# Optimization experiments

Measured on AMD Instinct MI355X. Metric: run time of the kernel, lower is better.

## Reference

```python
import jax, jax.numpy as jnp
import numpy as np

DEPTH = 4
EPS = 1e-5


def _bn(x, g, b):
    # training-mode BatchNorm over (B,H,W) per channel
    m = x.mean(axis=(0, 2, 3), keepdims=True)
    v = x.var(axis=(0, 2, 3), keepdims=True)
    return (x - m) * jax.lax.rsqrt(v + EPS) * g[None, :, None, None] + b[None, :, None, None]


def _conv_bn(x, w, g, b):
    # 1x1 conv (no bias) + BatchNorm
    y = jnp.einsum('bchw,oc->bohw', x, w)
    return _bn(y, g, b)


def _block_max_broadcast(x, gsz):
    # max over each (H/gsz, W/gsz) block of a gsz x gsz grid, broadcast back
    B, C, H, W = x.shape
    xr = x.reshape(B, C, gsz, H // gsz, gsz, W // gsz)
    m = xr.max(axis=(3, 5), keepdims=True)
    return jnp.broadcast_to(m, xr.shape).reshape(B, C, H, W)


def setup_inputs() -> dict:
    key = jax.random.key(0)
    ks = jax.random.split(key, 3)
    B, C, H, W = 4, 128, 256, 256
    x = jax.random.normal(ks[0], (B, C, H, W), dtype=jnp.float32)
    conv_w = jax.random.normal(ks[1], (DEPTH, C, C), dtype=jnp.float32) * 0.05
    conv_g = jnp.ones((DEPTH, C), dtype=jnp.float32)
    conv_b = jnp.zeros((DEPTH, C), dtype=jnp.float32)
    final_w = jax.random.normal(ks[2], (C, (DEPTH + 1) * C), dtype=jnp.float32) * 0.05
    final_g = jnp.ones((C,), dtype=jnp.float32)
    final_b = jnp.zeros((C,), dtype=jnp.float32)
    return {"x": x, "conv_w": conv_w, "conv_g": conv_g, "conv_b": conv_b,
            "final_w": final_w, "final_g": final_g, "final_b": final_b}


def reference(x, conv_w, conv_g, conv_b, final_w, final_g, final_b):
    # p[0]: identity; p[1+d]: block-max over 2^d x 2^d grid broadcast back, then 1x1 conv+BN
    p = [x]
    for d in range(DEPTH):
        pooled = _block_max_broadcast(x, 2 ** d)  # d=0 -> global max broadcast
        p.append(_conv_bn(pooled, conv_w[d], conv_g[d], conv_b[d]))
    out = jnp.concatenate(p, axis=1)  # [B, 5C, H, W]
    return _conv_bn(out, final_w, final_g, final_b)
```

## Files before the change

kernel.cpp:

```cpp
#include <hip/hip_runtime.h>
#include <hip/hip_bf16.h>
#include <math.h>
#include <float.h>

#define B_ 4
#define C_ 128
#define P_ 65536

#define M3_OFF      0
#define M2_OFF      32768
#define M1_OFF      40960
#define M0_OFF      43008
#define YBASE_      43520
#define SCALED_OFF  87040
#define SHIFTD_OFF  87552
#define CONTRIB_OFF 88064
#define S3_OFF      120832
#define SX_OFF      153600
#define G_OFF       154112
#define SCALEF_OFF  219648
#define SHIFTF_OFF  219776
#define MAXP_OFF    219904
#define SUMP_OFF    744192

using short8 = __attribute__((ext_vector_type(8))) short;
using f32x4 = __attribute__((ext_vector_type(4))) float;
using f32x16 = __attribute__((ext_vector_type(16))) float;

__device__ __forceinline__ int level_rel(int d) {
    return YBASE_ - 512 * (((1 << (2 * (d + 1))) - 1) / 3);
}

__device__ __forceinline__ unsigned int bfpair(float a, float b) {
    unsigned int ua = __float_as_uint(a), ub = __float_as_uint(b);
    ua = (ua + 0x7fffu + ((ua >> 16) & 1u)) >> 16;
    ub = (ub + 0x7fffu + ((ub >> 16) & 1u)) & 0xffff0000u;
    return ua | ub;
}

#define GLDS16(src, dst)                                                    \
    __builtin_amdgcn_global_load_lds(                                       \
        (const __attribute__((address_space(1))) unsigned int*)(src),       \
        (__attribute__((address_space(3))) unsigned int*)(dst), 16, 0, 0)

__global__ __launch_bounds__(256) void k_gram_pool(const float* __restrict__ x,
                                                   float* __restrict__ ws,
                                                   float* __restrict__ gpart) {
    __shared__ float tile[2][8192];
    int wg = blockIdx.x;
    int b = wg >> 7, rc = wg & 127;
    const float* xb = x + (size_t)b * C_ * P_ + (size_t)rc * 512;
    int t = threadIdx.x, l = t & 63, wv = t >> 6;
    int tr = (wv >> 1) * 64;
    int tcc = (wv & 1) * 64;
    bool doacc = ((wv & 1) == 0);

    f32x16 acc[2][2];
#pragma unroll
    for (int i = 0; i < 2; ++i)
#pragma unroll
        for (int j = 0; j < 2; ++j)
#pragma unroll
            for (int r = 0; r < 16; ++r) acc[i][j][r] = 0.f;
    float mxA[2][8], smA[2][8];
#pragma unroll
    for (int i = 0; i < 2; ++i)
#pragma unroll
        for (int j = 0; j < 8; ++j) { mxA[i][j] = -FLT_MAX; smA[i][j] = 0.f; }

#pragma unroll
    for (int i = 0; i < 8; ++i) {
        int row = wv * 32 + i * 4 + (l >> 4);
        int chunk = (l & 15) ^ (row & 15);
        GLDS16(xb + (size_t)row * P_ + chunk * 4, &tile[0][(wv * 32 + i * 4) * 64]);
    }
    __syncthreads();

#pragma unroll
    for (int s = 0; s < 8; ++s) {
        if (s < 7) {
#pragma unroll
            for (int i = 0; i < 8; ++i) {
                int row = wv * 32 + i * 4 + (l >> 4);
                int chunk = (l & 15) ^ (row & 15);
                GLDS16(xb + (size_t)row * P_ + (s + 1) * 64 + chunk * 4,
                       &tile[(s + 1) & 1][(wv * 32 + i * 4) * 64]);
            }
        }
        const float* tl = &tile[s & 1][0];
#pragma unroll
        for (int ks = 0; ks < 4; ++ks) {
            int jci = 2 * (s & 3) + (ks >> 1);
            int ch = ks * 4 + ((l >> 5) << 1);
            short8 fr[4];
#pragma unroll
            for (int fi = 0; fi < 4; ++fi) {
                int row = (fi < 2 ? tr : tcc) + (fi & 1) * 32 + (l & 31);
                int sw = row & 15;
                const float* p0 = tl + row * 64 + ((ch ^ sw) << 2);
                const float* p1 = tl + row * 64 + (((ch + 1) ^ sw) << 2);
                float4 v0 = *(const float4*)p0;
                float4 v1 = *(const float4*)p1;
                if (fi < 2 && doacc) {
                    mxA[fi][jci] = fmaxf(mxA[fi][jci],
                        fmaxf(fmaxf(fmaxf(v0.x, v0.y), fmaxf(v0.z, v0.w)),
                              fmaxf(fmaxf(v1.x, v1.y), fmaxf(v1.z, v1.w))));
                    smA[fi][jci] += ((v0.x + v0.y) + (v0.z + v0.w)) +
                                    ((v1.x + v1.y) + (v1.z + v1.w));
                }
                union { uint4 u; short8 s8; } cu;
                cu.u = make_uint4(bfpair(v0.x, v0.y), bfpair(v0.z, v0.w),
                                  bfpair(v1.x, v1.y), bfpair(v1.z, v1.w));
                fr[fi] = cu.s8;
            }
            acc[0][0] = __builtin_amdgcn_mfma_f32_32x32x16_bf16(fr[0], fr[2], acc[0][0], 0, 0, 0);
            acc[0][1] = __builtin_amdgcn_mfma_f32_32x32x16_bf16(fr[0], fr[3], acc[0][1], 0, 0, 0);
            acc[1][0] = __builtin_amdgcn_mfma_f32_32x32x16_bf16(fr[1], fr[2], acc[1][0], 0, 0, 0);
            acc[1][1] = __builtin_amdgcn_mfma_f32_32x32x16_bf16(fr[1], fr[3], acc[1][1], 0, 0, 0);
        }
        __syncthreads();
    }

    size_t gb = (size_t)wg * 16384;
#pragma unroll
    for (int i = 0; i < 2; ++i)
#pragma unroll
        for (int j = 0; j < 2; ++j)
#pragma unroll
            for (int r = 0; r < 16; ++r) {
                int row = tr + i * 32 + (r & 3) + 8 * (r >> 2) + 4 * (l >> 5);
                int col = tcc + j * 32 + (l & 31);
                gpart[gb + (size_t)row * 128 + col] = acc[i][j][r];
            }
    if (doacc) {
        int i3 = rc >> 4, rr = rc & 15;
#pragma unroll
        for (int half = 0; half < 2; ++half)
#pragma unroll
            for (int jc = 0; jc < 8; ++jc) {
                float m = mxA[half][jc], sv = smA[half][jc];
                m = fmaxf(m, __shfl_xor(m, 32));
                sv += __shfl_xor(sv, 32);
                if (l < 32) {
                    int c = tr + half * 32 + l;
                    size_t idx = ((size_t)(b * 128 + c) * 64 + i3 * 8 + jc) * 16 + rr;
                    ws[MAXP_OFF + idx] = m;
                    ws[SUMP_OFF + idx] = sv;
                }
            }
    }
}

__global__ __launch_bounds__(256) void k_reduceG(const float* __restrict__ gpart,
                                                 float* __restrict__ ws) {
    int tid = blockIdx.x * 256 + threadIdx.x;
    int b = tid >> 14, inner = tid & 16383;
    const float* p = gpart + (size_t)b * 128 * 16384 + inner;
    float s = 0.f;
    for (int r = 0; r < 128; ++r) s += p[(size_t)r * 16384];
    ws[G_OFF + tid] = s;
}

__global__ __launch_bounds__(256) void k_reduceMS(float* __restrict__ ws) {
    int bc = blockIdx.x;
    int t = threadIdx.x;
    int blk = t >> 2, q = t & 3;
    __shared__ float bm[64], bs[64];
    __shared__ float lv[24];
    __shared__ float sxr[8];
    {
        size_t base = (size_t)bc * 1024 + blk * 16 + q * 4;
        float4 mv = *(const float4*)(ws + MAXP_OFF + base);
        float4 sv = *(const float4*)(ws + SUMP_OFF + base);
        float m = fmaxf(fmaxf(mv.x, mv.y), fmaxf(mv.z, mv.w));
        float s = (sv.x + sv.y) + (sv.z + sv.w);
        m = fmaxf(m, __shfl_xor(m, 1)); s += __shfl_xor(s, 1);
        m = fmaxf(m, __shfl_xor(m, 2)); s += __shfl_xor(s, 2);
        if (q == 0) {
            bm[blk] = m;
            bs[blk] = s;
            ws[M3_OFF + (size_t)bc * 64 + blk] = m;
            ws[S3_OFF + (size_t)bc * 64 + blk] = s;
        }
    }
    __syncthreads();
    if (t < 8) {
        float sx = 0.f;
        for (int r = 0; r < 8; ++r) sx += bs[t * 8 + r];
        sxr[t] = sx;
    }
    if (t < 16) {
        int i2 = t >> 2, j2 = t & 3;
        float m = -FLT_MAX;
        for (int a = 0; a < 2; ++a)
            for (int b2 = 0; b2 < 2; ++b2)
                m = fmaxf(m, bm[(2 * i2 + a) * 8 + 2 * j2 + b2]);
        lv[t] = m;
        ws[M2_OFF + (size_t)bc * 16 + t] = m;
    }
    __syncthreads();
    if (t == 0) {
        float sx = 0.f;
        for (int r = 0; r < 8; ++r) sx += sxr[r];
        ws[SX_OFF + bc] = sx;
    }
    if (t < 4) {
        int i1 = t >> 1, j1 = t & 1;
        float m = -FLT_MAX;
        for (int a = 0; a < 2; ++a)
            for (int b2 = 0; b2 < 2; ++b2)
                m = fmaxf(m, lv[(2 * i1 + a) * 4 + 2 * j1 + b2]);
        lv[16 + t] = m;
        ws[M1_OFF + (size_t)bc * 4 + t] = m;
    }
    __syncthreads();
    if (t == 0)
        ws[M0_OFF + bc] = fmaxf(fmaxf(lv[16], lv[17]), fmaxf(lv[18], lv[19]));
}

__global__ __launch_bounds__(256) void k_conv_pool(const float* __restrict__ conv_w,
                                                   float* __restrict__ ws) {
    int bid = blockIdx.x;
    int d = bid >> 4, b = (bid >> 2) & 3, cchunk = bid & 3;
    int NB = 1 << (2 * d);
    int rel = level_rel(d);
    const float* Mb = ws + rel + (size_t)b * 128 * NB;
    float* Yb = ws + YBASE_ + rel + (size_t)b * 128 * NB;
    __shared__ float mlds[8192];
    int t = threadIdx.x;
    int tot = 128 * NB;
    for (int i = t; i < tot; i += 256) mlds[i] = Mb[i];
    __syncthreads();
    if (NB >= 4) {
        int nbq = NB >> 2;
        int nq = 32 * nbq;
        for (int qi = t; qi < nq; qi += 256) {
            int co = cchunk * 32 + (qi >> (2 * d - 2));
            int bq = qi & (nbq - 1);
            const float* wrow = conv_w + ((size_t)d * 128 + co) * 128;
            float a0 = 0.f, a1 = 0.f, a2 = 0.f, a3 = 0.f;
            for (int ci = 0; ci < 128; ++ci) {
                float4 mv = *(const float4*)(&mlds[ci * NB + bq * 4]);
                float wvv = wrow[ci];
                a0 = fmaf(wvv, mv.x, a0);
                a1 = fmaf(wvv, mv.y, a1);
                a2 = fmaf(wvv, mv.z, a2);
                a3 = fmaf(wvv, mv.w, a3);
            }
            float4 r;
            r.x = a0; r.y = a1; r.z = a2; r.w = a3;
            *(float4*)(&Yb[co * NB + bq * 4]) = r;
        }
    } else {
        for (int oi = t; oi < 32; oi += 256) {
            int co = cchunk * 32 + oi;
            const float* wrow = conv_w + (size_t)co * 128;
            float acc = 0.f;
            for (int ci = 0; ci < 128; ++ci) acc = fmaf(mlds[ci], wrow[ci], acc);
            Yb[co] = acc;
        }
    }
}

__global__ __launch_bounds__(256) void k_bnstats_d(const float* __restrict__ conv_g,
                                                   const float* __restrict__ conv_b,
                                                   float* __restrict__ ws) {
    int tid = blockIdx.x * 256 + threadIdx.x;
    if (tid >= 512) return;
    int d = tid >> 7, c = tid & 127;
    int NB = 1 << (2 * d);
    const float* Y = ws + YBASE_ + level_rel(d);
    int n = 4 * NB;
    float s = 0.f;
    for (int b = 0; b < 4; ++b)
        for (int k = 0; k < NB; ++k) s += Y[((size_t)b * 128 + c) * NB + k];
    float mean = s / (float)n;
    float v = 0.f;
    for (int b = 0; b < 4; ++b)
        for (int k = 0; k < NB; ++k) {
            float dd = Y[((size_t)b * 128 + c) * NB + k] - mean;
            v = fmaf(dd, dd, v);
        }
    float var = v / (float)n;
    float sc = conv_g[d * 128 + c] * rsqrtf(var + 1e-5f);
    ws[SCALED_OFF + tid] = sc;
    ws[SHIFTD_OFF + tid] = conv_b[d * 128 + c] - mean * sc;
}

__global__ __launch_bounds__(128) void k_contrib(const float* __restrict__ final_w,
                                                 float* __restrict__ ws) {
    int b = blockIdx.x >> 6, blk3 = blockIdx.x & 63;
    int i3 = blk3 >> 3, j3 = blk3 & 7;
    __shared__ float pn[512];
    int t = threadIdx.x;
    for (int k = t; k < 512; k += 128) {
        int d = k >> 7, c = k & 127;
        int sh = 3 - d;
        int blkd = (i3 >> sh) * (1 << d) + (j3 >> sh);
        int NB = 1 << (2 * d);
        float yv = ws[YBASE_ + level_rel(d) + ((size_t)b * 128 + c) * NB + blkd];
        pn[k] = yv * ws[SCALED_OFF + k] + ws[SHIFTD_OFF + k];
    }
    __syncthreads();
    const float* fw = final_w + (size_t)t * 640 + 128;
    float acc = 0.f;
#pragma unroll 8
    for (int k = 0; k < 512; k += 4) {
        float4 f = *(const float4*)(fw + k);
        acc = fmaf(pn[k], f.x, acc);
        acc = fmaf(pn[k + 1], f.y, acc);
        acc = fmaf(pn[k + 2], f.z, acc);
        acc = fmaf(pn[k + 3], f.w, acc);
    }
    ws[CONTRIB_OFF + ((size_t)b * 128 + t) * 64 + blk3] = acc;
}

__global__ __launch_bounds__(128) void k_stats(const float* __restrict__ final_w,
                                               const float* __restrict__ final_g,
                                               const float* __restrict__ final_b,
                                               float* __restrict__ ws) {
    int o = blockIdx.x, t = threadIdx.x;
    __shared__ __align__(16) float wlds[128];
    __shared__ __align__(16) float cvl[64];
    __shared__ float rbuf[4];
    wlds[t] = final_w[(size_t)o * 640 + t];
    __syncthreads();
    float SSQ = 0.f, SUM = 0.f;
    for (int b = 0; b < 4; ++b) {
        if (t < 64) cvl[t] = ws[CONTRIB_OFF + (size_t)(b * 128 + o) * 64 + t];
        __syncthreads();
        const float* Gb = ws + G_OFF + (size_t)b * 16384 + (size_t)t * 128;
        float a1 = 0.f;
#pragma unroll 8
        for (int k = 0; k < 128; k += 4) {
            float4 g = *(const float4*)(Gb + k);
            float4 w = *(const float4*)(&wlds[k]);
            a1 = fmaf(g.x, w.x, fmaf(g.y, w.y, fmaf(g.z, w.z, fmaf(g.w, w.w, a1))));
        }
        const float* S3p = ws + S3_OFF + (size_t)(b * 128 + t) * 64;
        float a2 = 0.f;
#pragma unroll 8
        for (int k = 0; k < 64; k += 4) {
            float4 sv = *(const float4*)(S3p + k);
            float4 cv = *(const float4*)(&cvl[k]);
            a2 = fmaf(sv.x, cv.x, fmaf(sv.y, cv.y, fmaf(sv.z, cv.z, fmaf(sv.w, cv.w, a2))));
        }
        float r1 = (a1 + 2.f * a2) * wlds[t];
        float r2 = wlds[t] * ws[SX_OFF + b * 128 + t];
        if (t < 64) {
            r1 += 1024.f * cvl[t] * cvl[t];
            r2 += 1024.f * cvl[t];
        }
#pragma unroll
        for (int k = 1; k < 64; k <<= 1) {
            r1 += __shfl_xor(r1, k);
            r2 += __shfl_xor(r2, k);
        }
        if ((t & 63) == 0) {
            rbuf[(t >> 6) * 2] = r1;
            rbuf[(t >> 6) * 2 + 1] = r2;
        }
        __syncthreads();
        SSQ += rbuf[0] + rbuf[2];
        SUM += rbuf[1] + rbuf[3];
        __syncthreads();
    }
    if (t == 0) {
        float mean = SUM / 262144.f;
        float var = SSQ / 262144.f - mean * mean;
        float sc = final_g[o] * rsqrtf(var + 1e-5f);
        ws[SCALEF_OFF + o] = sc;
        ws[SHIFTF_OFF + o] = final_b[o] - mean * sc;
    }
}

__global__ __launch_bounds__(256) void k_out(const float* __restrict__ x,
                                             const float* __restrict__ final_w,
                                             const float* __restrict__ ws,
                                             float* __restrict__ out) {
    __shared__ uint4 wtileq[2048];
    __shared__ float scl[128], shf[128], cvs[512];
    unsigned char* wtile = (unsigned char*)wtileq;
    int wgid = blockIdx.x;
    int b = wgid >> 9, pt = wgid & 511;
    int p0 = pt * 128;
    int t = threadIdx.x, l = t & 63, wv = t >> 6;
#pragma unroll
    for (int it = 0; it < 32; ++it) {
        int pid = it * 256 + t;
        int o = pid >> 6, cp = (pid & 63) * 2;
        float2 f = *(const float2*)(final_w + (size_t)o * 640 + cp);
        unsigned int u = bfpair(f.x, f.y);
        int wa = (o * 256 + cp * 2) ^ ((o & 7) << 4);
        *(unsigned int*)(wtile + wa) = u;
    }
    if (t < 128) {
        scl[t] = ws[SCALEF_OFF + t];
        shf[t] = ws[SHIFTF_OFF + t];
    }
    int i3 = pt >> 6, jb = (pt & 1) * 4;
    for (int q = t; q < 512; q += 256) {
        int o = q >> 2, jj = q & 3;
        cvs[q] = ws[CONTRIB_OFF + (size_t)(b * 128 + o) * 64 + i3 * 8 + jb + jj];
    }
    __syncthreads();

    const float* xb = x + (size_t)b * C_ * P_;
    int pw = p0 + wv * 32;
    f32x4 acc[8][2];
#pragma unroll
    for (int i = 0; i < 8; ++i) {
        acc[i][0] = (f32x4){0.f, 0.f, 0.f, 0.f};
        acc[i][1] = (f32x4){0.f, 0.f, 0.f, 0.f};
    }
#pragma unroll
    for (int ks = 0; ks < 4; ++ks) {
        short8 bf[2];
#pragma unroll
        for (int nt = 0; nt < 2; ++nt) {
            const float* xp = xb + (size_t)(ks * 32 + (l >> 4) * 8) * P_ + (pw + nt * 16 + (l & 15));
            float f0 = xp[0 * P_], f1 = xp[1 * P_], f2 = xp[2 * P_], f3 = xp[3 * P_];
            float f4 = xp[4 * P_], f5 = xp[5 * P_], f6 = xp[6 * P_], f7 = xp[7 * P_];
            union { uint4 u; short8 s; } cvtu;
            cvtu.u = make_uint4(bfpair(f0, f1), bfpair(f2, f3), bfpair(f4, f5), bfpair(f6, f7));
            bf[nt] = cvtu.s;
        }
#pragma unroll
        for (int mt = 0; mt < 8; ++mt) {
            int ra = ((mt * 16 + (l & 15)) * 256 + ks * 64 + (l >> 4) * 16) ^ ((l & 7) << 4);
            short8 af = *(const short8*)(wtile + ra);
            acc[mt][0] = __builtin_amdgcn_mfma_f32_16x16x32_bf16(af, bf[0], acc[mt][0], 0, 0, 0);
            acc[mt][1] = __builtin_amdgcn_mfma_f32_16x16x32_bf16(af, bf[1], acc[mt][1], 0, 0, 0);
        }
    }
#pragma unroll
    for (int mt = 0; mt < 8; ++mt)
#pragma unroll
        for (int nt = 0; nt < 2; ++nt) {
            int p = pw + nt * 16 + (l & 15);
            int jj = ((p & 255) >> 5) & 3;
#pragma unroll
            for (int r = 0; r < 4; ++r) {
                int o = mt * 16 + (l >> 4) * 4 + r;
                float z = acc[mt][nt][r] + cvs[o * 4 + jj];
                out[(size_t)(b * 128 + o) * P_ + p] = fmaf(z, scl[o], shf[o]);
            }
        }
}

extern "C" void kernel_launch(void* const* d_in, const int* in_sizes, int n_in,
                              void* d_out, int out_size, void* d_ws, size_t ws_size,
                              hipStream_t stream) {
    const float* x = (const float*)d_in[0];
    const float* conv_w = (const float*)d_in[1];
    const float* conv_g = (const float*)d_in[2];
    const float* conv_b = (const float*)d_in[3];
    const float* final_w = (const float*)d_in[4];
    const float* final_g = (const float*)d_in[5];
    const float* final_b = (const float*)d_in[6];
    float* out = (float*)d_out;
    float* ws = (float*)d_ws;

    k_gram_pool<<<512, 256, 0, stream>>>(x, ws, out);
    k_reduceG<<<256, 256, 0, stream>>>(out, ws);
    k_reduceMS<<<512, 256, 0, stream>>>(ws);
    k_conv_pool<<<64, 256, 0, stream>>>(conv_w, ws);
    k_bnstats_d<<<2, 256, 0, stream>>>(conv_g, conv_b, ws);
    k_contrib<<<B_ * 64, 128, 0, stream>>>(final_w, ws);
    k_stats<<<128, 128, 0, stream>>>(final_w, final_g, final_b, ws);
    k_out<<<2048, 256, 0, stream>>>(x, final_w, ws, out);
}
```

Before: 196.1 us.

## Use a four-slot LDS ring with three loads in flight in gram-pool kernel

Replaces the two-stage double buffer of 64-column tiles with a four-slot ring of 32-column tiles. Three tiles are prefetched ahead, and each step waits with explicit vmcnt counts and a single barrier instead of two syncthreads per step. The aim is to keep more global-to-LDS traffic in flight and hide memory latency behind the MFMA and reduction work. In exchange it doubles the number of pipeline steps and adds hand-tuned wait counts that must match the issue pattern exactly.

```diff
diff --git a/kernel.cpp b/kernel.cpp
--- a/kernel.cpp
+++ b/kernel.cpp
@@ -46,14 +46,15 @@
 __global__ __launch_bounds__(256) void k_gram_pool(const float* __restrict__ x,
                                                    float* __restrict__ ws,
                                                    float* __restrict__ gpart) {
-    __shared__ float tile[2][8192];
+    __shared__ float buf[4][4096];
     int wg = blockIdx.x;
     int b = wg >> 7, rc = wg & 127;
     const float* xb = x + (size_t)b * C_ * P_ + (size_t)rc * 512;
-    int t = threadIdx.x, l = t & 63, wv = t >> 6;
+    int t_ = threadIdx.x, l = t_ & 63, wv = t_ >> 6;
     int tr = (wv >> 1) * 64;
     int tcc = (wv & 1) * 64;
     bool doacc = ((wv & 1) == 0);
+    int lrow = l >> 3, lch = l & 7;
 
     f32x16 acc[2][2];
 #pragma unroll
@@ -68,45 +69,54 @@
 #pragma unroll
         for (int j = 0; j < 8; ++j) { mxA[i][j] = -FLT_MAX; smA[i][j] = 0.f; }
 
-#pragma unroll
-    for (int i = 0; i < 8; ++i) {
-        int row = wv * 32 + i * 4 + (l >> 4);
-        int chunk = (l & 15) ^ (row & 15);
-        GLDS16(xb + (size_t)row * P_ + chunk * 4, &tile[0][(wv * 32 + i * 4) * 64]);
-    }
-    __syncthreads();
-
-#pragma unroll
-    for (int s = 0; s < 8; ++s) {
-        if (s < 7) {
-#pragma unroll
-            for (int i = 0; i < 8; ++i) {
-                int row = wv * 32 + i * 4 + (l >> 4);
-                int chunk = (l & 15) ^ (row & 15);
-                GLDS16(xb + (size_t)row * P_ + (s + 1) * 64 + chunk * 4,
-                       &tile[(s + 1) & 1][(wv * 32 + i * 4) * 64]);
-            }
-        }
-        const float* tl = &tile[s & 1][0];
-#pragma unroll
-        for (int ks = 0; ks < 4; ++ks) {
-            int jci = 2 * (s & 3) + (ks >> 1);
+#define ISSUE(tt)                                                            \
+    do {                                                                     \
+        _Pragma("unroll") for (int i_ = 0; i_ < 4; ++i_) {                   \
+            int row_ = wv * 32 + i_ * 8 + lrow;                              \
+            int ch_ = lch ^ (row_ & 7);                                      \
+            GLDS16(xb + (size_t)row_ * P_ + (tt) * 32 + ch_ * 4,             \
+                   &buf[(tt) & 3][(wv * 32 + i_ * 8) * 32]);                 \
+        }                                                                    \
+    } while (0)
+
+    ISSUE(0);
+    ISSUE(1);
+    ISSUE(2);
+
+#pragma unroll
+    for (int t = 0; t < 16; ++t) {
+        if (t <= 13)
+            asm volatile("s_waitcnt vmcnt(8)" ::: "memory");
+        else if (t == 14)
+            asm volatile("s_waitcnt vmcnt(4)" ::: "memory");
+        else
+            asm volatile("s_waitcnt vmcnt(0)" ::: "memory");
+        __builtin_amdgcn_sched_barrier(0);
+        __builtin_amdgcn_s_barrier();
+        asm volatile("" ::: "memory");
+        __builtin_amdgcn_sched_barrier(0);
+        if (t + 3 < 16) ISSUE(t + 3);
+
+        const float* tl = &buf[t & 3][0];
+        int jc = t & 7;
+#pragma unroll
+        for (int ks = 0; ks < 2; ++ks) {
             int ch = ks * 4 + ((l >> 5) << 1);
             short8 fr[4];
 #pragma unroll
             for (int fi = 0; fi < 4; ++fi) {
                 int row = (fi < 2 ? tr : tcc) + (fi & 1) * 32 + (l & 31);
-                int sw = row & 15;
-                const float* p0 = tl + row * 64 + ((ch ^ sw) << 2);
-                const float* p1 = tl + row * 64 + (((ch + 1) ^ sw) << 2);
+                int sw = row & 7;
+                const float* p0 = tl + row * 32 + ((ch ^ sw) << 2);
+                const float* p1 = tl + row * 32 + (((ch + 1) ^ sw) << 2);
                 float4 v0 = *(const float4*)p0;
                 float4 v1 = *(const float4*)p1;
                 if (fi < 2 && doacc) {
-                    mxA[fi][jci] = fmaxf(mxA[fi][jci],
+                    mxA[fi][jc] = fmaxf(mxA[fi][jc],
                         fmaxf(fmaxf(fmaxf(v0.x, v0.y), fmaxf(v0.z, v0.w)),
                               fmaxf(fmaxf(v1.x, v1.y), fmaxf(v1.z, v1.w))));
-                    smA[fi][jci] += ((v0.x + v0.y) + (v0.z + v0.w)) +
-                                    ((v1.x + v1.y) + (v1.z + v1.w));
+                    smA[fi][jc] += ((v0.x + v0.y) + (v0.z + v0.w)) +
+                                   ((v1.x + v1.y) + (v1.z + v1.w));
                 }
                 union { uint4 u; short8 s8; } cu;
                 cu.u = make_uint4(bfpair(v0.x, v0.y), bfpair(v0.z, v0.w),
@@ -118,8 +128,8 @@
             acc[1][0] = __builtin_amdgcn_mfma_f32_32x32x16_bf16(fr[1], fr[2], acc[1][0], 0, 0, 0);
             acc[1][1] = __builtin_amdgcn_mfma_f32_32x32x16_bf16(fr[1], fr[3], acc[1][1], 0, 0, 0);
         }
-        __syncthreads();
-    }
+    }
+#undef ISSUE
 
     size_t gb = (size_t)wg * 16384;
 #pragma unroll
```

Result: no change. 196.1 us (-0.0%).
